# Performance work log

Measured on AMD Instinct MI355X. Metric: run time of the kernel, lower is better.

## Reference

```python
import jax, jax.numpy as jnp
import numpy as np
from math import sqrt


def setup_inputs() -> dict:
    key0 = jax.random.key(0)
    ks = jax.random.split(key0, 7)
    N, H, E, D, S = 32, 16, 128, 128, 2047
    return {
        "query": jax.random.normal(ks[0], (N, H, E), dtype=jnp.float32),
        "key": jax.random.normal(ks[1], (N, H, E), dtype=jnp.float32),
        "value": jax.random.normal(ks[2], (N, H, D), dtype=jnp.float32),
        "keys_cache": jax.random.normal(ks[3], (N, H, S, E), dtype=jnp.float32),
        "values_cache": jax.random.normal(ks[4], (N, H, S, D), dtype=jnp.float32),
        "w_pre": jax.random.normal(ks[5], (H, H), dtype=jnp.float32) * (1.0 / sqrt(H)),
        "w_post": jax.random.normal(ks[6], (H, H), dtype=jnp.float32) * (1.0 / sqrt(H)),
    }


def reference(query, key, value, keys_cache, values_cache, w_pre, w_post):
    # Single recurrent decode step with talking-heads mixing (dropout in eval mode).
    N, H, E = query.shape
    softmax_temp = 1.0 / sqrt(E)
    # Append current key/value to the cache: [N,H,S+1,E] / [N,H,S+1,D]
    keys = jnp.concatenate([keys_cache, key[:, :, None, :]], axis=2)
    values = jnp.concatenate([values_cache, value[:, :, None, :]], axis=2)
    # Scores: [N,H,S]
    QK = jnp.einsum('nhe,nhse->nhs', query, keys)
    # Pre-softmax talking heads (1x1 conv over head axis): out_g = sum_h w[g,h] * in_h
    QK = jnp.einsum('gh,nhs->ngs', w_pre, QK)
    A = jax.nn.softmax(softmax_temp * QK, axis=-1)
    # Post-softmax talking heads
    A = jnp.einsum('gh,nhs->ngs', w_post, A)
    # Weighted value readout: [N,H,D]
    V = jnp.einsum('nhs,nhsd->nhd', A, values)
    return V, keys, values
```

## Files before the change

kernel.cpp:

```cpp
#include <hip/hip_runtime.h>
#include <cstddef>

constexpr int N_  = 32;
constexpr int H_  = 16;
constexpr int E_  = 128;
constexpr int D_  = 128;
constexpr int S_  = 2047;
constexpr int SP1 = 2048;
constexpr int NH  = N_ * H_;

constexpr int ROWS_PER_BLOCK = 256;
constexpr int CHUNKS = SP1 / ROWS_PER_BLOCK;
constexpr int COLCH  = SP1 / 256;

typedef float vfloat4 __attribute__((ext_vector_type(4)));

__global__ __launch_bounds__(256) void k1_keys_scores(
    const float* __restrict__ query, const float* __restrict__ key,
    const float* __restrict__ keys_cache,
    float* __restrict__ keys_out, float* __restrict__ scores)
{
  __shared__ float sc[ROWS_PER_BLOCK];
  const int bid   = blockIdx.x;
  const int nh    = bid / CHUNKS;
  const int chunk = bid % CHUNKS;
  const int tid   = threadIdx.x;
  const int wave  = tid >> 6;
  const int lane  = tid & 63;
  const int half  = lane >> 5;
  const int lcol  = lane & 31;

  const vfloat4 q4 = *reinterpret_cast<const vfloat4*>(query + (size_t)nh * E_ + lcol * 4);

  #pragma unroll 8
  for (int it = 0; it < ROWS_PER_BLOCK / 8; ++it) {
    const int r = it * 8 + wave * 2 + half;
    const int s = chunk * ROWS_PER_BLOCK + r;
    const float* src = (s < S_) ? (keys_cache + ((size_t)nh * S_ + s) * E_)
                                : (key + (size_t)nh * E_);
    vfloat4 k4 = *reinterpret_cast<const vfloat4*>(src + lcol * 4);
    __builtin_nontemporal_store(k4,
        reinterpret_cast<vfloat4*>(keys_out + ((size_t)nh * SP1 + s) * E_ + lcol * 4));

    float p = q4.x * k4.x + q4.y * k4.y + q4.z * k4.z + q4.w * k4.w;
    p += __shfl_xor(p, 1);
    p += __shfl_xor(p, 2);
    p += __shfl_xor(p, 4);
    p += __shfl_xor(p, 8);
    p += __shfl_xor(p, 16);
    if (lcol == 0) sc[r] = p;
  }
  __syncthreads();
  scores[(size_t)nh * SP1 + chunk * ROWS_PER_BLOCK + tid] = sc[tid];
}

__global__ __launch_bounds__(256) void k2a_stats(
    const float* __restrict__ scores, const float* __restrict__ w_pre,
    float* __restrict__ blkstats)
{
  __shared__ float wp[H_ * H_];
  __shared__ float red[4][H_];
  __shared__ float bmax[H_];
  const int n   = blockIdx.x >> 3;
  const int cc  = blockIdx.x & 7;
  const int tid = threadIdx.x;
  const int wave = tid >> 6;
  const int lane = tid & 63;
  const float temp = 0.08838834764831845f;

  wp[tid] = w_pre[tid];
  __syncthreads();

  const float* base = scores + (size_t)n * H_ * SP1 + cc * 256 + tid;
  float sc[H_];
  #pragma unroll
  for (int h = 0; h < H_; ++h) sc[h] = base[(size_t)h * SP1];

  float mx[H_];
  #pragma unroll
  for (int g = 0; g < H_; ++g) {
    float acc = 0.0f;
    #pragma unroll
    for (int h = 0; h < H_; ++h) acc += wp[g * H_ + h] * sc[h];
    mx[g] = acc * temp;
  }

  #pragma unroll
  for (int g = 0; g < H_; ++g) {
    float v = mx[g];
    #pragma unroll
    for (int m = 1; m <= 32; m <<= 1) v = fmaxf(v, __shfl_xor(v, m));
    if (lane == 0) red[wave][g] = v;
  }
  __syncthreads();
  if (tid < H_) {
    float v = fmaxf(fmaxf(red[0][tid], red[1][tid]), fmaxf(red[2][tid], red[3][tid]));
    bmax[tid] = v;
    blkstats[((size_t)(n * COLCH + cc) * 2 + 0) * H_ + tid] = v;
  }
  __syncthreads();

  #pragma unroll
  for (int g = 0; g < H_; ++g) {
    float e = __expf(mx[g] - bmax[g]);
    #pragma unroll
    for (int m = 1; m <= 32; m <<= 1) e += __shfl_xor(e, m);
    if (lane == 0) red[wave][g] = e;
  }
  __syncthreads();
  if (tid < H_) {
    blkstats[((size_t)(n * COLCH + cc) * 2 + 1) * H_ + tid] =
        red[0][tid] + red[1][tid] + red[2][tid] + red[3][tid];
  }
}

__global__ __launch_bounds__(256) void k2c_a2(
    const float* __restrict__ scores, const float* __restrict__ blkstats,
    const float* __restrict__ w_pre, const float* __restrict__ w_post,
    float* __restrict__ a2out)
{
  __shared__ float wp[H_ * H_];
  __shared__ float wq[H_ * H_];
  __shared__ float mg[H_];
  __shared__ float ig[H_];
  const int n   = blockIdx.x >> 3;
  const int cc  = blockIdx.x & 7;
  const int tid = threadIdx.x;
  const float temp = 0.08838834764831845f;

  wp[tid] = w_pre[tid];
  wq[tid] = w_post[tid];
  if (tid < H_) {
    float bm[COLCH], bs[COLCH];
    #pragma unroll
    for (int c = 0; c < COLCH; ++c) {
      bm[c] = blkstats[((size_t)(n * COLCH + c) * 2 + 0) * H_ + tid];
      bs[c] = blkstats[((size_t)(n * COLCH + c) * 2 + 1) * H_ + tid];
    }
    float m = bm[0];
    #pragma unroll
    for (int c = 1; c < COLCH; ++c) m = fmaxf(m, bm[c]);
    float den = 0.0f;
    #pragma unroll
    for (int c = 0; c < COLCH; ++c) den += bs[c] * __expf(bm[c] - m);
    mg[tid] = m;
    ig[tid] = 1.0f / den;
  }
  __syncthreads();

  const float* base = scores + (size_t)n * H_ * SP1 + cc * 256 + tid;
  float sc[H_];
  #pragma unroll
  for (int h = 0; h < H_; ++h) sc[h] = base[(size_t)h * SP1];

  float P[H_];
  #pragma unroll
  for (int h = 0; h < H_; ++h) {
    float acc = 0.0f;
    #pragma unroll
    for (int h2 = 0; h2 < H_; ++h2) acc += wp[h * H_ + h2] * sc[h2];
    P[h] = __expf(acc * temp - mg[h]) * ig[h];
  }

  #pragma unroll
  for (int g = 0; g < H_; ++g) {
    float a = 0.0f;
    #pragma unroll
    for (int h = 0; h < H_; ++h) a += wq[g * H_ + h] * P[h];
    a2out[((size_t)(n * H_ + g)) * SP1 + cc * 256 + tid] = a;
  }
}

__global__ __launch_bounds__(256) void k3_values(
    const float* __restrict__ value, const float* __restrict__ values_cache,
    const float* __restrict__ a2buf, float* __restrict__ values_out,
    float* __restrict__ partials)
{
  __shared__ float lds[8][128];
  __shared__ float a2[ROWS_PER_BLOCK];
  const int bid   = blockIdx.x;
  const int nh    = bid / CHUNKS;
  const int chunk = bid % CHUNKS;
  const int tid   = threadIdx.x;
  const int wave  = tid >> 6;
  const int lane  = tid & 63;
  const int half  = lane >> 5;
  const int lcol  = lane & 31;
  const int group = wave * 2 + half;

  a2[tid] = a2buf[(size_t)nh * SP1 + chunk * ROWS_PER_BLOCK + tid];
  __syncthreads();

  float accx = 0.0f, accy = 0.0f, accz = 0.0f, accw = 0.0f;

  #pragma unroll 8
  for (int it = 0; it < ROWS_PER_BLOCK / 8; ++it) {
    const int r = it * 8 + wave * 2 + half;
    const int s = chunk * ROWS_PER_BLOCK + r;
    const float* src = (s < S_) ? (values_cache + ((size_t)nh * S_ + s) * D_)
                                : (value + (size_t)nh * D_);
    vfloat4 v4 = *reinterpret_cast<const vfloat4*>(src + lcol * 4);
    __builtin_nontemporal_store(v4,
        reinterpret_cast<vfloat4*>(values_out + ((size_t)nh * SP1 + s) * D_ + lcol * 4));

    const float w = a2[r];
    accx += w * v4.x;
    accy += w * v4.y;
    accz += w * v4.z;
    accw += w * v4.w;
  }

  lds[group][lcol * 4 + 0] = accx;
  lds[group][lcol * 4 + 1] = accy;
  lds[group][lcol * 4 + 2] = accz;
  lds[group][lcol * 4 + 3] = accw;
  __syncthreads();
  if (tid < 128) {
    float sum = 0.0f;
    #pragma unroll
    for (int gq = 0; gq < 8; ++gq) sum += lds[gq][tid];
    partials[(size_t)bid * 128 + tid] = sum;
  }
}

__global__ __launch_bounds__(256) void k4_reduce(
    const float* __restrict__ partials, float* __restrict__ v_out)
{
  const int g = blockIdx.x * 256 + threadIdx.x;
  const int nh = g >> 7;
  const int d = g & 127;
  float s = 0.0f;
  #pragma unroll
  for (int c = 0; c < CHUNKS; ++c)
    s += partials[((size_t)(nh * CHUNKS + c)) * 128 + d];
  v_out[g] = s;
}

extern "C" void kernel_launch(void* const* d_in, const int* in_sizes, int n_in,
                              void* d_out, int out_size, void* d_ws, size_t ws_size,
                              hipStream_t stream) {
  const float* query        = (const float*)d_in[0];
  const float* key          = (const float*)d_in[1];
  const float* value        = (const float*)d_in[2];
  const float* keys_cache   = (const float*)d_in[3];
  const float* values_cache = (const float*)d_in[4];
  const float* w_pre        = (const float*)d_in[5];
  const float* w_post       = (const float*)d_in[6];

  float* out = (float*)d_out;
  float* v_out      = out;
  float* keys_out   = out + (size_t)NH * D_;
  float* values_out = keys_out + (size_t)NH * SP1 * E_;

  float* buf0     = (float*)d_ws;
  float* a2buf    = buf0 + (size_t)NH * SP1;
  float* blkstats = a2buf + (size_t)NH * SP1;
  float* partials = blkstats + (size_t)N_ * COLCH * 2 * H_;

  k1_keys_scores<<<NH * CHUNKS, 256, 0, stream>>>(query, key, keys_cache,
                                                  keys_out, buf0);
  k2a_stats<<<N_ * COLCH, 256, 0, stream>>>(buf0, w_pre, blkstats);
  k2c_a2<<<N_ * COLCH, 256, 0, stream>>>(buf0, blkstats, w_pre, w_post, a2buf);
  k3_values<<<NH * CHUNKS, 256, 0, stream>>>(value, values_cache, a2buf,
                                             values_out, partials);
  k4_reduce<<<(NH * 128) / 256, 256, 0, stream>>>(partials, v_out);
}
```

Measured before the change: 446.3 us.

## Fuse softmax stats and A2 kernels with intra-grid barrier; last-block reduce in k3

Merges the two softmax kernels into one. Blocks of the same batch publish their partial max and sum, then spin on a per-batch atomic counter until all eight column chunks arrive, which removes a launch and the reload and recomputation of mixed scores. The final partial reduction is folded into the values kernel using a last-block-done counter, which removes the k4 launch. This adds a memset, atomics, and a spin wait that relies on all 256 blocks of k2 being co-resident, otherwise it could deadlock.

```diff
diff --git a/kernel.cpp b/kernel.cpp
--- a/kernel.cpp
+++ b/kernel.cpp
@@ -54,13 +54,17 @@
   scores[(size_t)nh * SP1 + chunk * ROWS_PER_BLOCK + tid] = sc[tid];
 }
 
-__global__ __launch_bounds__(256) void k2a_stats(
+__global__ __launch_bounds__(256) void k2_fused(
     const float* __restrict__ scores, const float* __restrict__ w_pre,
-    float* __restrict__ blkstats)
+    const float* __restrict__ w_post, float* __restrict__ a2out,
+    float* __restrict__ stats, int* __restrict__ ctr)
 {
   __shared__ float wp[H_ * H_];
+  __shared__ float wq[H_ * H_];
   __shared__ float red[4][H_];
   __shared__ float bmax[H_];
+  __shared__ float mg[H_];
+  __shared__ float ig[H_];
   const int n   = blockIdx.x >> 3;
   const int cc  = blockIdx.x & 7;
   const int tid = threadIdx.x;
@@ -69,6 +73,7 @@
   const float temp = 0.08838834764831845f;
 
   wp[tid] = w_pre[tid];
+  wq[tid] = w_post[tid];
   __syncthreads();
 
   const float* base = scores + (size_t)n * H_ * SP1 + cc * 256 + tid;
@@ -93,11 +98,9 @@
     if (lane == 0) red[wave][g] = v;
   }
   __syncthreads();
-  if (tid < H_) {
-    float v = fmaxf(fmaxf(red[0][tid], red[1][tid]), fmaxf(red[2][tid], red[3][tid]));
-    bmax[tid] = v;
-    blkstats[((size_t)(n * COLCH + cc) * 2 + 0) * H_ + tid] = v;
-  }
+  if (tid < H_)
+    bmax[tid] = fmaxf(fmaxf(red[0][tid], red[1][tid]),
+                      fmaxf(red[2][tid], red[3][tid]));
   __syncthreads();
 
   #pragma unroll
@@ -108,34 +111,31 @@
     if (lane == 0) red[wave][g] = e;
   }
   __syncthreads();
+
   if (tid < H_) {
-    blkstats[((size_t)(n * COLCH + cc) * 2 + 1) * H_ + tid] =
-        red[0][tid] + red[1][tid] + red[2][tid] + red[3][tid];
-  }
-}
-
-__global__ __launch_bounds__(256) void k2c_a2(
-    const float* __restrict__ scores, const float* __restrict__ blkstats,
-    const float* __restrict__ w_pre, const float* __restrict__ w_post,
-    float* __restrict__ a2out)
-{
-  __shared__ float wp[H_ * H_];
-  __shared__ float wq[H_ * H_];
-  __shared__ float mg[H_];
-  __shared__ float ig[H_];
-  const int n   = blockIdx.x >> 3;
-  const int cc  = blockIdx.x & 7;
-  const int tid = threadIdx.x;
-  const float temp = 0.08838834764831845f;
-
-  wp[tid] = w_pre[tid];
-  wq[tid] = w_post[tid];
+    const float bsum = red[0][tid] + red[1][tid] + red[2][tid] + red[3][tid];
+    __hip_atomic_store(&stats[((size_t)(n * COLCH + cc) * 2 + 0) * H_ + tid],
+                       bmax[tid], __ATOMIC_RELAXED, __HIP_MEMORY_SCOPE_AGENT);
+    __hip_atomic_store(&stats[((size_t)(n * COLCH + cc) * 2 + 1) * H_ + tid],
+                       bsum, __ATOMIC_RELAXED, __HIP_MEMORY_SCOPE_AGENT);
+  }
+  __syncthreads();
+
+  if (tid == 0) {
+    __hip_atomic_fetch_add(&ctr[n], 1, __ATOMIC_RELEASE, __HIP_MEMORY_SCOPE_AGENT);
+    while (__hip_atomic_load(&ctr[n], __ATOMIC_ACQUIRE, __HIP_MEMORY_SCOPE_AGENT) < COLCH)
+      __builtin_amdgcn_s_sleep(1);
+  }
+  __syncthreads();
+
   if (tid < H_) {
     float bm[COLCH], bs[COLCH];
     #pragma unroll
     for (int c = 0; c < COLCH; ++c) {
-      bm[c] = blkstats[((size_t)(n * COLCH + c) * 2 + 0) * H_ + tid];
-      bs[c] = blkstats[((size_t)(n * COLCH + c) * 2 + 1) * H_ + tid];
+      bm[c] = __hip_atomic_load(&stats[((size_t)(n * COLCH + c) * 2 + 0) * H_ + tid],
+                                __ATOMIC_RELAXED, __HIP_MEMORY_SCOPE_AGENT);
+      bs[c] = __hip_atomic_load(&stats[((size_t)(n * COLCH + c) * 2 + 1) * H_ + tid],
+                                __ATOMIC_RELAXED, __HIP_MEMORY_SCOPE_AGENT);
     }
     float m = bm[0];
     #pragma unroll
@@ -148,19 +148,10 @@
   }
   __syncthreads();
 
-  const float* base = scores + (size_t)n * H_ * SP1 + cc * 256 + tid;
-  float sc[H_];
-  #pragma unroll
-  for (int h = 0; h < H_; ++h) sc[h] = base[(size_t)h * SP1];
-
   float P[H_];
   #pragma unroll
-  for (int h = 0; h < H_; ++h) {
-    float acc = 0.0f;
-    #pragma unroll
-    for (int h2 = 0; h2 < H_; ++h2) acc += wp[h * H_ + h2] * sc[h2];
-    P[h] = __expf(acc * temp - mg[h]) * ig[h];
-  }
+  for (int h = 0; h < H_; ++h)
+    P[h] = __expf(mx[h] - mg[h]) * ig[h];
 
   #pragma unroll
   for (int g = 0; g < H_; ++g) {
@@ -174,10 +165,12 @@
 __global__ __launch_bounds__(256) void k3_values(
     const float* __restrict__ value, const float* __restrict__ values_cache,
     const float* __restrict__ a2buf, float* __restrict__ values_out,
-    float* __restrict__ partials)
+    float* __restrict__ partials, int* __restrict__ ctr,
+    float* __restrict__ v_out)
 {
   __shared__ float lds[8][128];
   __shared__ float a2[ROWS_PER_BLOCK];
+  __shared__ int lastflag;
   const int bid   = blockIdx.x;
   const int nh    = bid / CHUNKS;
   const int chunk = bid % CHUNKS;
@@ -219,21 +212,26 @@
     float sum = 0.0f;
     #pragma unroll
     for (int gq = 0; gq < 8; ++gq) sum += lds[gq][tid];
-    partials[(size_t)bid * 128 + tid] = sum;
-  }
-}
-
-__global__ __launch_bounds__(256) void k4_reduce(
-    const float* __restrict__ partials, float* __restrict__ v_out)
-{
-  const int g = blockIdx.x * 256 + threadIdx.x;
-  const int nh = g >> 7;
-  const int d = g & 127;
-  float s = 0.0f;
-  #pragma unroll
-  for (int c = 0; c < CHUNKS; ++c)
-    s += partials[((size_t)(nh * CHUNKS + c)) * 128 + d];
-  v_out[g] = s;
+    __hip_atomic_store(&partials[(size_t)bid * 128 + tid], sum,
+                       __ATOMIC_RELAXED, __HIP_MEMORY_SCOPE_AGENT);
+  }
+  __syncthreads();
+
+  if (tid == 0) {
+    const int old = __hip_atomic_fetch_add(&ctr[nh], 1, __ATOMIC_ACQ_REL,
+                                           __HIP_MEMORY_SCOPE_AGENT);
+    lastflag = (old == CHUNKS - 1);
+  }
+  __syncthreads();
+
+  if (lastflag && tid < 128) {
+    float s = 0.0f;
+    #pragma unroll
+    for (int c = 0; c < CHUNKS; ++c)
+      s += __hip_atomic_load(&partials[((size_t)(nh * CHUNKS + c)) * 128 + tid],
+                             __ATOMIC_RELAXED, __HIP_MEMORY_SCOPE_AGENT);
+    v_out[(size_t)nh * 128 + tid] = s;
+  }
 }
 
 extern "C" void kernel_launch(void* const* d_in, const int* in_sizes, int n_in,
@@ -254,14 +252,17 @@
 
   float* buf0     = (float*)d_ws;
   float* a2buf    = buf0 + (size_t)NH * SP1;
-  float* blkstats = a2buf + (size_t)NH * SP1;
-  float* partials = blkstats + (size_t)N_ * COLCH * 2 * H_;
+  float* stats    = a2buf + (size_t)NH * SP1;
+  float* partials = stats + (size_t)N_ * COLCH * 2 * H_;
+  int*   ctrs     = (int*)(partials + (size_t)NH * CHUNKS * 128);
+
+  hipMemsetAsync(ctrs, 0, (N_ + NH) * sizeof(int), stream);
 
   k1_keys_scores<<<NH * CHUNKS, 256, 0, stream>>>(query, key, keys_cache,
                                                   keys_out, buf0);
-  k2a_stats<<<N_ * COLCH, 256, 0, stream>>>(buf0, w_pre, blkstats);
-  k2c_a2<<<N_ * COLCH, 256, 0, stream>>>(buf0, blkstats, w_pre, w_post, a2buf);
+  k2_fused<<<N_ * COLCH, 256, 0, stream>>>(buf0, w_pre, w_post, a2buf,
+                                           stats, ctrs);
   k3_values<<<NH * CHUNKS, 256, 0, stream>>>(value, values_cache, a2buf,
-                                             values_out, partials);
-  k4_reduce<<<(NH * 128) / 256, 256, 0, stream>>>(partials, v_out);
-}
+                                             values_out, partials,
+                                             ctrs + N_, v_out);
+}
```

Measured after the change: 692.2 us. +55.1%, slower.
